# Kernel tuning notes

Measured on AMD Instinct MI355X. Metric: run time of the kernel, lower is better.

## Reference

```python
import jax, jax.numpy as jnp
import numpy as np

N = 50000
E = 800000
D = 64


def setup_inputs() -> dict:
    key = jax.random.key(0)
    ks = jax.random.split(key, 6)
    s = 1.0 / np.sqrt(D)
    return {
        "x": jax.random.normal(ks[0], (N, D), dtype=jnp.float32),
        "edge_index": jax.random.randint(ks[1], (2, E), 0, N, dtype=jnp.int64),
        "W_l1": jax.random.normal(ks[2], (D, D), dtype=jnp.float32) * s,
        "b_l1": jnp.zeros((D,), dtype=jnp.float32),
        "W_r1": jax.random.normal(ks[3], (D, D), dtype=jnp.float32) * s,
        "W_l2": jax.random.normal(ks[4], (D, D), dtype=jnp.float32) * s,
        "b_l2": jnp.zeros((D,), dtype=jnp.float32),
        "W_r2": jax.random.normal(ks[5], (D, D), dtype=jnp.float32) * s,
    }


def _sage_conv(x, src, dst, W_l, b_l, W_r):
    # PyG SAGEConv (aggr='mean'): out = lin_l(mean_{j in N(i)} x_j) + lin_r(x_i)
    msgs = x[src]                                   # [E, D] gather
    agg = jax.ops.segment_sum(msgs, dst, num_segments=N)          # [N, D]
    cnt = jax.ops.segment_sum(jnp.ones((src.shape[0],), x.dtype), dst,
                              num_segments=N)                      # [N]
    agg = agg / jnp.maximum(cnt, 1.0)[:, None]       # mean with deg>=1 guard
    return agg @ W_l.T + b_l + x @ W_r.T


def reference(x, edge_index, W_l1, b_l1, W_r1, W_l2, b_l2, W_r2):
    src, dst = edge_index[0], edge_index[1]
    h = jnp.tanh(_sage_conv(x, src, dst, W_l1, b_l1, W_r1))
    out = _sage_conv(h, src, dst, W_l2, b_l2, W_r2)
    return out
```

## Files before the change

### kernel.cpp

```cpp
#include <hip/hip_runtime.h>
#include <hip/hip_bf16.h>

#define D 64
#define NS 32
#define NQ 4

typedef __attribute__((ext_vector_type(8))) short bf16x8;
typedef __attribute__((ext_vector_type(4))) float f32x4;

struct Rec {
    unsigned char off[NS];
    int rptr;
    int pad[7];
};

__device__ __forceinline__ float bf2f(unsigned short u) {
    return __uint_as_float(((unsigned)u) << 16);
}
__device__ __forceinline__ unsigned short f2bf(float f) {
    __hip_bfloat16 b = __float2bfloat16(f);
    return *(unsigned short*)&b;
}


__global__ void prep_k(const float* __restrict__ x, unsigned short* __restrict__ xbf,
                       const float* __restrict__ Wl1, const float* __restrict__ Wr1,
                       const float* __restrict__ Wl2, const float* __restrict__ Wr2,
                       unsigned short* __restrict__ Wbf,
                       int* __restrict__ done, int n4) {
    int i = blockIdx.x * blockDim.x + threadIdx.x;
    if (i < n4) {
        float4 v = ((const float4*)x)[i];
        ushort4 u;
        u.x = f2bf(v.x); u.y = f2bf(v.y); u.z = f2bf(v.z); u.w = f2bf(v.w);
        ((ushort4*)xbf)[i] = u;
    }
    if (i == 0) *done = 0;
    if (i < 4096) {
        Wbf[i]           = f2bf(Wl1[i]);
        Wbf[4096 + i]    = f2bf(Wr1[i]);
        Wbf[8192 + i]    = f2bf(Wl2[i]);
        Wbf[12288 + i]   = f2bf(Wr2[i]);
    }
}


__global__ __launch_bounds__(1024) void histA_k(
    const int* __restrict__ dst, unsigned char* __restrict__ posL,
    unsigned short* __restrict__ cntT, int N, int E, int SS, int HS)
{
    __shared__ int hist32[6256];
    const int s = blockIdx.x >> 2;
    const int q = blockIdx.x & 3;
    const int nbase = q * HS;
    const int nrel  = min(N - nbase, HS);
    const int words = (nrel + 1) >> 1;
    for (int i = threadIdx.x; i < words; i += 1024) hist32[i] = 0;
    __syncthreads();

    const int ebeg = s * SS, eend = min(E, ebeg + SS);
    int e0 = ebeg + threadIdx.x * 4;
    for (; e0 + 4 <= eend; e0 += 4096) {
        int4 dv = *(const int4*)(dst + e0);
        int d[4] = {dv.x, dv.y, dv.z, dv.w};
        #pragma unroll
        for (int i = 0; i < 4; ++i) {
            int r = d[i] - nbase;
            if (r >= 0 && r < nrel) {
                int sh  = (r & 1) << 4;
                int old = atomicAdd(&hist32[r >> 1], 1 << sh);
                posL[e0 + i] = (unsigned char)((old >> sh) & 0xff);
            }
        }
    }
    for (int e = e0; e < eend; ++e) {
        int r = dst[e] - nbase;
        if (r >= 0 && r < nrel) {
            int sh  = (r & 1) << 4;
            int old = atomicAdd(&hist32[r >> 1], 1 << sh);
            posL[e] = (unsigned char)((old >> sh) & 0xff);
        }
    }
    __syncthreads();
    for (int i = threadIdx.x; i < words; i += 1024) {
        int u  = hist32[i];
        int n0 = nbase + 2 * i;
        cntT[(size_t)n0 * NS + s] = (unsigned short)(u & 0xffff);
        if (2 * i + 1 < nrel)
            cntT[(size_t)(n0 + 1) * NS + s] = (unsigned short)(u >> 16);
    }
}

__global__ void combine_k(const unsigned short* __restrict__ cntT,
                          Rec* __restrict__ record, int* __restrict__ rowptrL,
                          int* __restrict__ bsum, int* __restrict__ done,
                          int N, int NB)
{
    __shared__ int tmp[256];
    __shared__ int islast;
    int gid = blockIdx.x * 256 + threadIdx.x;
    unsigned int wrd[16];
    unsigned int offw[8] = {0,0,0,0,0,0,0,0};
    int total = 0;
    if (gid < N) {
        const uint4* p = (const uint4*)(cntT + (size_t)gid * NS);
        uint4 a = p[0], b = p[1], c = p[2], d = p[3];
        wrd[0]=a.x; wrd[1]=a.y; wrd[2]=a.z; wrd[3]=a.w;
        wrd[4]=b.x; wrd[5]=b.y; wrd[6]=b.z; wrd[7]=b.w;
        wrd[8]=c.x; wrd[9]=c.y; wrd[10]=c.z; wrd[11]=c.w;
        wrd[12]=d.x; wrd[13]=d.y; wrd[14]=d.z; wrd[15]=d.w;
        #pragma unroll
        for (int s = 0; s < NS; ++s) {
            int cnt_s = (wrd[s >> 1] >> ((s & 1) * 16)) & 0xffff;
            offw[s >> 2] |= ((unsigned int)(total & 0xff)) << ((s & 3) * 8);
            total += cnt_s;
        }
    }
    tmp[threadIdx.x] = total;
    __syncthreads();
    for (int off = 1; off < 256; off <<= 1) {
        int t = (threadIdx.x >= off) ? tmp[threadIdx.x - off] : 0;
        __syncthreads();
        tmp[threadIdx.x] += t;
        __syncthreads();
    }
    int excl = tmp[threadIdx.x] - total;
    if (gid < N) {
        rowptrL[gid] = excl;
        int4* pr = (int4*)&record[gid];
        pr[0] = make_int4((int)offw[0], (int)offw[1], (int)offw[2], (int)offw[3]);
        pr[1] = make_int4((int)offw[4], (int)offw[5], (int)offw[6], (int)offw[7]);
        pr[2] = make_int4(excl, 0, 0, 0);
    }
    if (threadIdx.x == 255) {
        atomicExch(&bsum[blockIdx.x], tmp[255]);
        __threadfence();
        int prev = atomicAdd(done, 1);
        islast = (prev == NB - 1) ? 1 : 0;
    }
    __syncthreads();
    if (islast) {
        int b = (threadIdx.x < NB) ? atomicAdd(&bsum[threadIdx.x], 0) : 0;
        tmp[threadIdx.x] = b;
        __syncthreads();
        for (int off = 1; off < 256; off <<= 1) {
            int t = (threadIdx.x >= off) ? tmp[threadIdx.x - off] : 0;
            __syncthreads();
            tmp[threadIdx.x] += t;
            __syncthreads();
        }
        if (threadIdx.x < NB)
            atomicExch(&bsum[threadIdx.x], tmp[threadIdx.x] - b);
    }
}

__global__ void fill3_k(const int* __restrict__ src, const int* __restrict__ dst,
                        const unsigned char* __restrict__ posL,
                        const Rec* __restrict__ record, const int* __restrict__ bsum,
                        unsigned short* __restrict__ col, int E, int SS) {
    int e0 = (blockIdx.x * blockDim.x + threadIdx.x) * 4;
    if (e0 + 4 <= E) {
        int4 dd = *(const int4*)(dst + e0);
        int4 ss = *(const int4*)(src + e0);
        uchar4 p = *(const uchar4*)(posL + e0);
        int d[4] = {dd.x, dd.y, dd.z, dd.w};
        int sc[4] = {ss.x, ss.y, ss.z, ss.w};
        unsigned char pp[4] = {p.x, p.y, p.z, p.w};
        #pragma unroll
        for (int i = 0; i < 4; ++i) {
            int e = e0 + i;
            int sl = e / SS;
            const Rec* r = &record[d[i]];
            int slot = r->rptr + bsum[d[i] >> 8] + (int)r->off[sl] + (int)pp[i];
            col[slot] = (unsigned short)sc[i];
        }
    } else {
        for (int e = e0; e < E; ++e) {
            int dv = dst[e];
            const Rec* r = &record[dv];
            col[r->rptr + bsum[dv >> 8] + (int)r->off[e / SS] + (int)posL[e]] =
                (unsigned short)src[e];
        }
    }
}


__device__ __forceinline__ float tanh_fast(float v) {
    float e = __expf(2.f * v);
    return 1.f - 2.f * __builtin_amdgcn_rcpf(e + 1.f);
}

template <int TANH>
__global__ __launch_bounds__(256) void layer_k(
    const unsigned short* __restrict__ xb,
    const int* __restrict__ rowptrL, const int* __restrict__ bsum,
    const unsigned short* __restrict__ col,
    const unsigned short* __restrict__ Wlb,
    const unsigned short* __restrict__ Wrb,
    const float* __restrict__ bias,
    float* __restrict__ outf, unsigned short* __restrict__ outb, int N, int E)
{
    __shared__ unsigned short sagg[16][72];
    const int tid = threadIdx.x;
    const int idx = tid & 15;
    const int nl  = tid >> 4;
    const int n0  = blockIdx.x * 16;
    const int n   = n0 + nl;

    if (n < N) {
        const int beg = rowptrL[n] + bsum[n >> 8];
        const int end = (n + 1 < N) ? (rowptrL[n + 1] + bsum[(n + 1) >> 8]) : E;
        float ax[8], ay[8], az[8], aw[8];
        #pragma unroll
        for (int s = 0; s < 8; ++s) { ax[s]=0.f; ay[s]=0.f; az[s]=0.f; aw[s]=0.f; }
        for (int j = beg; j < end; j += 8) {
            #pragma unroll
            for (int s = 0; s < 8; ++s) {
                int jj = j + s;
                float m = (jj < end) ? 1.f : 0.f;
                jj = (jj < end) ? jj : end - 1;
                int c = col[jj];
                ushort4 u = *(const ushort4*)(xb + (size_t)c * D + idx * 4);
                ax[s] = fmaf(m, bf2f(u.x), ax[s]);
                ay[s] = fmaf(m, bf2f(u.y), ay[s]);
                az[s] = fmaf(m, bf2f(u.z), az[s]);
                aw[s] = fmaf(m, bf2f(u.w), aw[s]);
            }
        }
        float sx = ((ax[0]+ax[1])+(ax[2]+ax[3]))+((ax[4]+ax[5])+(ax[6]+ax[7]));
        float sy = ((ay[0]+ay[1])+(ay[2]+ay[3]))+((ay[4]+ay[5])+(ay[6]+ay[7]));
        float sz = ((az[0]+az[1])+(az[2]+az[3]))+((az[4]+az[5])+(az[6]+az[7]));
        float sw = ((aw[0]+aw[1])+(aw[2]+aw[3]))+((aw[4]+aw[5])+(aw[6]+aw[7]));
        const float inv = 1.0f / fmaxf((float)(end - beg), 1.0f);
        ushort4 o;
        o.x = f2bf(sx*inv); o.y = f2bf(sy*inv); o.z = f2bf(sz*inv); o.w = f2bf(sw*inv);
        *(ushort4*)&sagg[nl][idx * 4] = o;
    } else {
        *(ushort4*)&sagg[nl][idx * 4] = make_ushort4(0, 0, 0, 0);
    }
    __syncthreads();

    const int lane = tid & 63;
    const int wid  = tid >> 6;
    const int fr   = lane & 15;
    const int k0   = (lane >> 4) * 8;
    const int f    = wid * 16 + fr;

    bf16x8 bl[2], br[2];
    {
        const unsigned short* pl = Wlb + f * 64 + k0;
        const unsigned short* pr = Wrb + f * 64 + k0;
        #pragma unroll
        for (int kc = 0; kc < 2; ++kc) {
            bl[kc] = *(const bf16x8*)(pl + kc * 32);
            br[kc] = *(const bf16x8*)(pr + kc * 32);
        }
    }
    float bv = bias[f];
    f32x4 acc = (f32x4){bv, bv, bv, bv};

    bf16x8 aa[2], axf[2];
    #pragma unroll
    for (int kc = 0; kc < 2; ++kc)
        aa[kc] = *(const bf16x8*)&sagg[fr][kc * 32 + k0];
    {
        const unsigned short* px = xb + (size_t)(n0 + fr) * D + k0;
        #pragma unroll
        for (int kc = 0; kc < 2; ++kc)
            axf[kc] = *(const bf16x8*)(px + kc * 32);
    }

    #pragma unroll
    for (int kc = 0; kc < 2; ++kc) {
        acc = __builtin_amdgcn_mfma_f32_16x16x32_bf16(aa[kc],  bl[kc], acc, 0, 0, 0);
        acc = __builtin_amdgcn_mfma_f32_16x16x32_bf16(axf[kc], br[kc], acc, 0, 0, 0);
    }

    const int rbase = n0 + (lane >> 4) * 4;
    #pragma unroll
    for (int r = 0; r < 4; ++r) {
        int node = rbase + r;
        if (node < N) {
            float v = acc[r];
            if (TANH) {
                v = tanh_fast(v);
                outb[(size_t)node * D + f] = f2bf(v);
            } else {
                outf[(size_t)node * D + f] = v;
            }
        }
    }
}


extern "C" void kernel_launch(void* const* d_in, const int* in_sizes, int n_in,
                              void* d_out, int out_size, void* d_ws, size_t ws_size,
                              hipStream_t stream) {
    const float* x   = (const float*)d_in[0];
    const int*   ei  = (const int*)d_in[1];
    const float* Wl1 = (const float*)d_in[2];
    const float* bl1 = (const float*)d_in[3];
    const float* Wr1 = (const float*)d_in[4];
    const float* Wl2 = (const float*)d_in[5];
    const float* bl2 = (const float*)d_in[6];
    const float* Wr2 = (const float*)d_in[7];

    const int N = in_sizes[0] / D;
    const int E = in_sizes[1] / 2;
    const int* srcI = ei;
    const int* dstI = ei + E;

    const int SS = (E + NS - 1) / NS;
    const int HS = (N + NQ - 1) / NQ;

    auto al = [](size_t v) { return (v + 255) & ~(size_t)255; };
    char* w = (char*)d_ws;
    size_t off = 0;
    int*            rowptrL = (int*)(w + off);            off += al((size_t)N * 4);
    int*            bsum    = (int*)(w + off);            off += al(1024);
    int*            done    = (int*)(w + off);            off += al(256);
    unsigned short* colA    = (unsigned short*)(w + off); off += al((size_t)E * 2);
    unsigned char*  posL    = (unsigned char*)(w + off);  off += al((size_t)E);
    unsigned short* cntT    = (unsigned short*)(w + off); off += al((size_t)N * NS * 2);
    Rec*            record  = (Rec*)(w + off);            off += al((size_t)N * sizeof(Rec));
    unsigned short* xbf     = (unsigned short*)(w + off); off += al((size_t)N * D * 2);
    unsigned short* hbf     = (unsigned short*)(w + off); off += al((size_t)N * D * 2);
    unsigned short* Wbf     = (unsigned short*)(w + off); off += al((size_t)4 * D * D * 2);
    unsigned short* Wb_l1 = Wbf, *Wb_r1 = Wbf + D*D, *Wb_l2 = Wbf + 2*D*D, *Wb_r2 = Wbf + 3*D*D;

    float* out = (float*)d_out;

    const int NB  = (N + 255) / 256;
    const int EB4 = (E / 4 + 255) / 256;
    const int PB  = (N * D / 4 + 255) / 256;
    const int LB  = (N + 15) / 16;

    prep_k<<<PB, 256, 0, stream>>>(x, xbf, Wl1, Wr1, Wl2, Wr2, Wbf, done, N * D / 4);
    histA_k<<<NS * NQ, 1024, 0, stream>>>(dstI, posL, cntT, N, E, SS, HS);
    combine_k<<<NB, 256, 0, stream>>>(cntT, record, rowptrL, bsum, done, N, NB);
    fill3_k<<<EB4, 256, 0, stream>>>(srcI, dstI, posL, record, bsum, colA, E, SS);

    layer_k<1><<<LB, 256, 0, stream>>>(xbf, rowptrL, bsum, colA, Wb_l1, Wb_r1, bl1,
                                       nullptr, hbf, N, E);
    layer_k<0><<<LB, 256, 0, stream>>>(hbf, rowptrL, bsum, colA, Wb_l2, Wb_r2, bl2,
                                       out, nullptr, N, E);
}
```

Before: 115.4 us.

## Make each wavefront own four nodes to drop the block-wide barrier

Each 64-lane wavefront now aggregates neighbours for its own four nodes and keeps them in a private LDS slice, which removes the __syncthreads between the gather and matmul phases. Each wave then computes all 64 output features with four MFMA tiles, replicating its four node rows across the sixteen MFMA rows. The aim is to let waves move from gather to matmul without waiting on slower waves in the block. In exchange, MFMA work and weight-register loads per wave grow fourfold, and output stores come from only sixteen lanes. The self-feature row index is now clamped to N-1.

After: 143.2 us. 1.24x slower.

```diff
diff --git a/kernel.cpp b/kernel.cpp
--- a/kernel.cpp
+++ b/kernel.cpp
@@ -200,12 +200,14 @@
     const float* __restrict__ bias,
     float* __restrict__ outf, unsigned short* __restrict__ outb, int N, int E)
 {
-    __shared__ unsigned short sagg[16][72];
-    const int tid = threadIdx.x;
-    const int idx = tid & 15;
-    const int nl  = tid >> 4;
-    const int n0  = blockIdx.x * 16;
-    const int n   = n0 + nl;
+    __shared__ unsigned short sagg[4][4][72];
+    const int tid  = threadIdx.x;
+    const int wid  = tid >> 6;
+    const int lane = tid & 63;
+    const int idx  = lane & 15;
+    const int nl   = lane >> 4;
+    const int n0   = blockIdx.x * 16 + wid * 4;
+    const int n    = n0 + nl;
 
     if (n < N) {
         const int beg = rowptrL[n] + bsum[n >> 8];
@@ -234,59 +236,68 @@
         const float inv = 1.0f / fmaxf((float)(end - beg), 1.0f);
         ushort4 o;
         o.x = f2bf(sx*inv); o.y = f2bf(sy*inv); o.z = f2bf(sz*inv); o.w = f2bf(sw*inv);
-        *(ushort4*)&sagg[nl][idx * 4] = o;
+        *(ushort4*)&sagg[wid][nl][idx * 4] = o;
     } else {
-        *(ushort4*)&sagg[nl][idx * 4] = make_ushort4(0, 0, 0, 0);
-    }
-    __syncthreads();
-
-    const int lane = tid & 63;
-    const int wid  = tid >> 6;
-    const int fr   = lane & 15;
-    const int k0   = (lane >> 4) * 8;
-    const int f    = wid * 16 + fr;
-
-    bf16x8 bl[2], br[2];
-    {
-        const unsigned short* pl = Wlb + f * 64 + k0;
-        const unsigned short* pr = Wrb + f * 64 + k0;
-        #pragma unroll
-        for (int kc = 0; kc < 2; ++kc) {
-            bl[kc] = *(const bf16x8*)(pl + kc * 32);
-            br[kc] = *(const bf16x8*)(pr + kc * 32);
-        }
-    }
-    float bv = bias[f];
-    f32x4 acc = (f32x4){bv, bv, bv, bv};
+        *(ushort4*)&sagg[wid][nl][idx * 4] = make_ushort4(0, 0, 0, 0);
+    }
+
+    const int fr = lane & 15;
+    const int k0 = (lane >> 4) * 8;
+    const int nr = fr & 3;
 
     bf16x8 aa[2], axf[2];
     #pragma unroll
     for (int kc = 0; kc < 2; ++kc)
-        aa[kc] = *(const bf16x8*)&sagg[fr][kc * 32 + k0];
+        aa[kc] = *(const bf16x8*)&sagg[wid][nr][kc * 32 + k0];
     {
-        const unsigned short* px = xb + (size_t)(n0 + fr) * D + k0;
+        const unsigned short* px = xb + (size_t)min(n0 + nr, N - 1) * D + k0;
         #pragma unroll
         for (int kc = 0; kc < 2; ++kc)
             axf[kc] = *(const bf16x8*)(px + kc * 32);
     }
 
+    bf16x8 bl[4][2], br[4][2];
     #pragma unroll
-    for (int kc = 0; kc < 2; ++kc) {
-        acc = __builtin_amdgcn_mfma_f32_16x16x32_bf16(aa[kc],  bl[kc], acc, 0, 0, 0);
-        acc = __builtin_amdgcn_mfma_f32_16x16x32_bf16(axf[kc], br[kc], acc, 0, 0, 0);
-    }
-
-    const int rbase = n0 + (lane >> 4) * 4;
+    for (int t = 0; t < 4; ++t) {
+        const unsigned short* pl = Wlb + (t * 16 + fr) * 64 + k0;
+        const unsigned short* pr = Wrb + (t * 16 + fr) * 64 + k0;
+        #pragma unroll
+        for (int kc = 0; kc < 2; ++kc) {
+            bl[t][kc] = *(const bf16x8*)(pl + kc * 32);
+            br[t][kc] = *(const bf16x8*)(pr + kc * 32);
+        }
+    }
+
+    f32x4 acc[4];
     #pragma unroll
-    for (int r = 0; r < 4; ++r) {
-        int node = rbase + r;
-        if (node < N) {
-            float v = acc[r];
-            if (TANH) {
-                v = tanh_fast(v);
-                outb[(size_t)node * D + f] = f2bf(v);
-            } else {
-                outf[(size_t)node * D + f] = v;
+    for (int t = 0; t < 4; ++t) {
+        float b = bias[t * 16 + fr];
+        acc[t] = (f32x4){b, b, b, b};
+    }
+    #pragma unroll
+    for (int t = 0; t < 4; ++t) {
+        #pragma unroll
+        for (int kc = 0; kc < 2; ++kc) {
+            acc[t] = __builtin_amdgcn_mfma_f32_16x16x32_bf16(aa[kc],  bl[t][kc], acc[t], 0, 0, 0);
+            acc[t] = __builtin_amdgcn_mfma_f32_16x16x32_bf16(axf[kc], br[t][kc], acc[t], 0, 0, 0);
+        }
+    }
+
+    if (lane < 16) {
+        #pragma unroll
+        for (int r = 0; r < 4; ++r) {
+            int node = n0 + r;
+            if (node < N) {
+                #pragma unroll
+                for (int t = 0; t < 4; ++t) {
+                    float v = acc[t][r];
+                    if (TANH) {
+                        v = tanh_fast(v);
+                        outb[(size_t)node * D + t * 16 + lane] = f2bf(v);
+                    } else {
+                        outf[(size_t)node * D + t * 16 + lane] = v;
+                    }
+                }
             }
         }
     }
```
